# Kernel optimization log

Measured on AMD Instinct MI355X. Metric: run time of the kernel, lower is better.

Reference implementation:

```python
import jax, jax.numpy as jnp
import numpy as np

D = 768
H = 12
DH = D // H
DFF = 4 * D
B, S = 2, 2048


def setup_inputs() -> dict:
    key = jax.random.key(0)
    ks = jax.random.split(key, 12)
    inp = {
        "X": jax.random.normal(ks[0], (B, S, D), dtype=jnp.float32),
        # per-head projections, stacked over heads (nn.Linear: y = x W^T + b; we store W already transposed as [d, d_h])
        "Wq": jax.random.normal(ks[1], (H, D, DH), dtype=jnp.float32) * (1.0 / np.sqrt(D)),
        "bq": jnp.zeros((H, DH), dtype=jnp.float32),
        "Wk": jax.random.normal(ks[2], (H, D, DH), dtype=jnp.float32) * (1.0 / np.sqrt(D)),
        "bk": jnp.zeros((H, DH), dtype=jnp.float32),
        "Wv": jax.random.normal(ks[3], (H, D, DH), dtype=jnp.float32) * (1.0 / np.sqrt(D)),
        "bv": jnp.zeros((H, DH), dtype=jnp.float32),
        "W0": jax.random.normal(ks[4], (D, D), dtype=jnp.float32) * (1.0 / np.sqrt(D)),
        "b0": jnp.zeros((D,), dtype=jnp.float32),
        # FFN params are torch.randn (unit std) in the original
        "W1": jax.random.normal(ks[5], (D, DFF), dtype=jnp.float32),
        "b1": jnp.zeros((DFF,), dtype=jnp.float32),
        "W2": jax.random.normal(ks[6], (DFF, D), dtype=jnp.float32),
        "b2": jnp.zeros((D,), dtype=jnp.float32),
        "g1": jnp.ones((D,), dtype=jnp.float32),
        "o1": jnp.zeros((D,), dtype=jnp.float32),
        "g2": jnp.ones((D,), dtype=jnp.float32),
        "o2": jnp.zeros((D,), dtype=jnp.float32),
    }
    return inp


def _layernorm(x, gain, offset):
    # original: (x - mean) / (std + 1e-5)  with population std (unbiased=False)
    m = jnp.mean(x, axis=-1, keepdims=True)
    sd = jnp.sqrt(jnp.mean((x - m) ** 2, axis=-1, keepdims=True))
    return gain * ((x - m) / (sd + 1e-5)) + offset


def _mha(x, Wq, bq, Wk, bk, Wv, bv, W0, b0):
    # batched over heads; equivalent to the per-head SHA loop + concat
    q = jnp.einsum("bsd,hdk->bhsk", x, Wq) + bq[None, :, None, :]
    k = jnp.einsum("bsd,hdk->bhsk", x, Wk) + bk[None, :, None, :]
    v = jnp.einsum("bsd,hdk->bhsk", x, Wv) + bv[None, :, None, :]
    scores = jnp.einsum("bhsk,bhtk->bhst", q, k) / np.sqrt(DH).astype(np.float32)
    seq = x.shape[1]
    causal = jnp.tril(jnp.ones((seq, seq), dtype=bool))
    scores = jnp.where(causal[None, None], scores, -jnp.inf)
    w = jax.nn.softmax(scores, axis=-1)
    out = jnp.einsum("bhst,bhtk->bhsk", w, v)
    out = jnp.transpose(out, (0, 2, 1, 3)).reshape(x.shape[0], seq, D)  # concat heads
    return out @ W0 + b0


def reference(X, Wq, bq, Wk, bk, Wv, bv, W0, b0, W1, b1, W2, b2, g1, o1, g2, o2):
    h = X + _mha(_layernorm(X, g1, o1), Wq, bq, Wk, bk, Wv, bv, W0, b0)
    y = _layernorm(h, g2, o2)
    y = jnp.maximum(y @ W1 + b1, 0.0) @ W2 + b2
    return h + y
```

## Files before the change

### kernel.cpp

```cpp
#include <hip/hip_runtime.h>
#include <hip/hip_bf16.h>
#include <cstdint>

#define BB 2
#define SS 2048
#define DD 768
#define HH 12
#define DHH 64
#define DFF 3072
#define MM (BB * SS)

typedef __attribute__((ext_vector_type(8))) short bf16x8;
typedef __attribute__((ext_vector_type(4))) float f32x4;
typedef __attribute__((ext_vector_type(16))) float f32x16;
typedef __attribute__((ext_vector_type(4))) unsigned short u16x4;
typedef __attribute__((ext_vector_type(8))) unsigned short u16x8;
typedef unsigned int u32;

#define DEV static __device__ __forceinline__

typedef __attribute__((address_space(1))) void AS1void;
typedef __attribute__((address_space(3))) void AS3void;

DEV void async_copy16(const void* g, void* l) {
  __builtin_amdgcn_global_load_lds((AS1void*)g, (AS3void*)l, 16, 0, 0);
}

DEV unsigned short bf16bits(float f) {
  __hip_bfloat16 h = __float2bfloat16(f);
  return *(unsigned short*)&h;
}

DEV float bits2f(unsigned short u) {
  u32 x = ((u32)u) << 16;
  union { u32 u; float f; } c; c.u = x;
  return c.f;
}

DEV u32 pack2(float a, float b) {
  return ((u32)bf16bits(b) << 16) | (u32)bf16bits(a);
}

__global__ __launch_bounds__(256) void prolog_kernel(
    const float* __restrict__ Wq, const float* __restrict__ Wk,
    const float* __restrict__ Wv, const float* __restrict__ bq,
    const float* __restrict__ bk, const float* __restrict__ bv,
    __hip_bfloat16* __restrict__ WqkvT, float* __restrict__ qkvbias,
    const float* __restrict__ W0, const float* __restrict__ W1,
    const float* __restrict__ W2, __hip_bfloat16* __restrict__ W0T,
    __hip_bfloat16* __restrict__ W1T, __hip_bfloat16* __restrict__ W2T,
    const float* __restrict__ X, const float* __restrict__ g1,
    const float* __restrict__ o1, __hip_bfloat16* __restrict__ ln1)
{
  __shared__ float tile[64][65];
  const int bid = blockIdx.x;

  if (bid < 432) {
    const int y = bid % 12, z = bid / 12;
    const int p = z / HH, h = z - p * HH;
    const float* in = (p == 0 ? Wq : (p == 1 ? Wk : Wv)) + (size_t)h * DD * DHH;
    const int r0 = y * 64;
    if (y == 0 && threadIdx.x < DHH) {
      const float* bsrc = (p == 0 ? bq : (p == 1 ? bk : bv));
      qkvbias[p * DD + h * DHH + threadIdx.x] = bsrc[h * DHH + threadIdx.x];
    }
    for (int i = threadIdx.x; i < 4096; i += 256) {
      int r = i >> 6, c = i & 63;
      tile[r][c] = in[(size_t)(r0 + r) * DHH + c];
    }
    __syncthreads();
    for (int i = threadIdx.x; i < 4096; i += 256) {
      int c = i >> 6, r = i & 63;
      WqkvT[(size_t)(p * DD + h * DHH + c) * DD + r0 + r] = __float2bfloat16(tile[r][c]);
    }
  } else if (bid < 1728) {
    int id = bid - 432;
    const float* in; __hip_bfloat16* out; int R, C, xt, yt;
    if (id < 144)      { in = W0; out = W0T; R = DD;  C = DD;  xt = id % 12; yt = id / 12; }
    else if (id < 720) { id -= 144; in = W1; out = W1T; R = DD;  C = DFF; xt = id % 48; yt = id / 48; }
    else               { id -= 720; in = W2; out = W2T; R = DFF; C = DD;  xt = id % 12; yt = id / 12; }
    const int c0 = xt * 64, r0 = yt * 64;
    for (int i = threadIdx.x; i < 4096; i += 256) {
      int r = i >> 6, c = i & 63;
      tile[r][c] = in[(size_t)(r0 + r) * C + c0 + c];
    }
    __syncthreads();
    for (int i = threadIdx.x; i < 4096; i += 256) {
      int c = i >> 6, r = i & 63;
      out[(size_t)(c0 + c) * R + r0 + r] = __float2bfloat16(tile[r][c]);
    }
  } else {
    const int wave = threadIdx.x >> 6;
    const int lane = threadIdx.x & 63;
    const int row = (bid - 1728) * 4 + wave;
    const float* xr = X + (size_t)row * DD;

    float4 v[3];
    float s1 = 0.f, s2 = 0.f;
#pragma unroll
    for (int j = 0; j < 3; ++j) {
      v[j] = *(const float4*)(xr + (j * 64 + lane) * 4);
      s1 += v[j].x + v[j].y + v[j].z + v[j].w;
      s2 += v[j].x * v[j].x + v[j].y * v[j].y + v[j].z * v[j].z + v[j].w * v[j].w;
    }
#pragma unroll
    for (int d = 1; d < 64; d <<= 1) {
      s1 += __shfl_xor(s1, d);
      s2 += __shfl_xor(s2, d);
    }
    const float mean = s1 * (1.0f / 768.0f);
    const float var = fmaxf(s2 * (1.0f / 768.0f) - mean * mean, 0.0f);
    const float rs = 1.0f / (sqrtf(var) + 1e-5f);

    unsigned short* orow = (unsigned short*)ln1 + (size_t)row * DD;
#pragma unroll
    for (int j = 0; j < 3; ++j) {
      const int c = (j * 64 + lane) * 4;
      float4 g4 = *(const float4*)(g1 + c);
      float4 o4 = *(const float4*)(o1 + c);
      u16x4 pk;
      pk[0] = bf16bits(g4.x * ((v[j].x - mean) * rs) + o4.x);
      pk[1] = bf16bits(g4.y * ((v[j].y - mean) * rs) + o4.y);
      pk[2] = bf16bits(g4.z * ((v[j].z - mean) * rs) + o4.z);
      pk[3] = bf16bits(g4.w * ((v[j].w - mean) * rs) + o4.w);
      *(u16x4*)(orow + c) = pk;
    }
  }
}

__global__ __launch_bounds__(256) void kvimg_kernel(
    const __hip_bfloat16* __restrict__ qkv, char* __restrict__ kimg,
    char* __restrict__ vimg)
{
  __shared__ unsigned short tileK[64][72];
  __shared__ unsigned short tileV[64][72];
  const int bh = blockIdx.y;
  const int b = bh / HH, h = bh - (bh / HH) * HH;
  const int t0 = blockIdx.x * 64;
  const int HD = 3 * DD;
  const unsigned short* Kp = (const unsigned short*)qkv + (size_t)(b * SS) * HD + DD + h * DHH;
  const unsigned short* Vp = (const unsigned short*)qkv + (size_t)(b * SS) * HD + 2 * DD + h * DHH;
  char* kdst = kimg + ((size_t)bh * 32 + blockIdx.x) * 8192;
  char* vdst = vimg + ((size_t)bh * 32 + blockIdx.x) * 8192;

  for (int i = threadIdx.x; i < 512; i += 256) {
    const int r = i >> 3, c8 = (i & 7) * 8;
    *(bf16x8*)&tileK[r][c8] = *(const bf16x8*)(Kp + (size_t)(t0 + r) * HD + c8);
    *(bf16x8*)&tileV[r][c8] = *(const bf16x8*)(Vp + (size_t)(t0 + r) * HD + c8);
  }
  __syncthreads();
  for (int i = threadIdx.x; i < 512; i += 256) {
    const int f = i >> 6, l = i & 63;
    const int kc = f >> 1, half = f & 1;
    const int lc = l & 31, lh = l >> 5;
    *(bf16x8*)(kdst + i * 16) = *(const bf16x8*)&tileK[half * 32 + lc][kc * 16 + lh * 8];
    union { unsigned short u[8]; bf16x8 v; } w;
#pragma unroll
    for (int e = 0; e < 8; ++e) w.u[e] = tileV[kc * 16 + lh * 8 + e][half * 32 + lc];
    *(bf16x8*)(vdst + i * 16) = w.v;
  }
}

template<bool RELU, bool OUT_BF16, bool HAS_RES>
__global__ __launch_bounds__(256) void gemm_bt(
    const __hip_bfloat16* __restrict__ A, const __hip_bfloat16* __restrict__ BT,
    const float* __restrict__ bias, const float* __restrict__ res,
    void* __restrict__ outp, int M, int N, int K)
{
  __shared__ __hip_bfloat16 Alds[2][128 * 32];
  __shared__ __hip_bfloat16 Blds[2][128 * 32];
  const int tid = threadIdx.x;
  const int wave = tid >> 6;
  const int lane = tid & 63;
  const int fr = lane & 15, fq = lane >> 4;
  const int wr = wave >> 1, wc = wave & 1;
  const int bm = blockIdx.y * 128, bn = blockIdx.x * 128;

  const int srow = tid >> 2;
  const int scol = (tid & 3) * 8;
  const __hip_bfloat16* ag0 = A + (size_t)(bm + srow) * K + scol;
  const __hip_bfloat16* ag1 = A + (size_t)(bm + 64 + srow) * K + scol;
  const __hip_bfloat16* bg0 = BT + (size_t)(bn + srow) * K + scol;
  const __hip_bfloat16* bg1 = BT + (size_t)(bn + 64 + srow) * K + scol;
  const int so = wave * 512;

  f32x4 acc[4][4] = {};

  async_copy16(ag0, &Alds[0][so]);
  async_copy16(ag1, &Alds[0][2048 + so]);
  async_copy16(bg0, &Blds[0][so]);
  async_copy16(bg1, &Blds[0][2048 + so]);
  __syncthreads();

  const int niter = K / 32;
  for (int i = 0; i < niter; ++i) {
    const int cur = i & 1;
    if (i + 1 < niter) {
      const int k1 = (i + 1) * 32;
      async_copy16(ag0 + k1, &Alds[cur ^ 1][so]);
      async_copy16(ag1 + k1, &Alds[cur ^ 1][2048 + so]);
      async_copy16(bg0 + k1, &Blds[cur ^ 1][so]);
      async_copy16(bg1 + k1, &Blds[cur ^ 1][2048 + so]);
    }
    bf16x8 af[4], bfr[4];
#pragma unroll
    for (int i4 = 0; i4 < 4; ++i4)
      af[i4] = *(const bf16x8*)(&Alds[cur][(wr * 64 + i4 * 16 + fr) * 32 + fq * 8]);
#pragma unroll
    for (int j4 = 0; j4 < 4; ++j4)
      bfr[j4] = *(const bf16x8*)(&Blds[cur][(wc * 64 + j4 * 16 + fr) * 32 + fq * 8]);
#pragma unroll
    for (int i4 = 0; i4 < 4; ++i4)
#pragma unroll
      for (int j4 = 0; j4 < 4; ++j4)
        acc[i4][j4] = __builtin_amdgcn_mfma_f32_16x16x32_bf16(af[i4], bfr[j4], acc[i4][j4], 0, 0, 0);
    __syncthreads();
  }

#pragma unroll
  for (int j = 0; j < 4; ++j) {
    const int c = bn + wc * 64 + j * 16 + fr;
    const float bv = bias[c];
#pragma unroll
    for (int i = 0; i < 4; ++i) {
#pragma unroll
      for (int r = 0; r < 4; ++r) {
        const int rr = bm + wr * 64 + i * 16 + fq * 4 + r;
        float v = acc[i][j][r] + bv;
        if (RELU) v = fmaxf(v, 0.0f);
        if (HAS_RES) v += res[(size_t)rr * N + c];
        if (OUT_BF16) ((__hip_bfloat16*)outp)[(size_t)rr * N + c] = __float2bfloat16(v);
        else          ((float*)outp)[(size_t)rr * N + c] = v;
      }
    }
  }
}

__global__ __launch_bounds__(256) void gemm_bt_sk(
    const __hip_bfloat16* __restrict__ A, const __hip_bfloat16* __restrict__ BT,
    unsigned short* __restrict__ part01, unsigned short* __restrict__ part23,
    int M, int N, int K, int K_per)
{
  __shared__ __hip_bfloat16 Alds[2][128 * 32];
  __shared__ __hip_bfloat16 Blds[2][128 * 32];
  const int tid = threadIdx.x;
  const int wave = tid >> 6;
  const int lane = tid & 63;
  const int fr = lane & 15, fq = lane >> 4;
  const int wr = wave >> 1, wc = wave & 1;
  const int bm = blockIdx.y * 128, bn = blockIdx.x * 128;
  const int z = blockIdx.z;
  unsigned short* part = (z < 2 ? part01 : part23) + (size_t)(z & 1) * M * N;
  const int kbase = z * K_per;

  const int srow = tid >> 2;
  const int scol = (tid & 3) * 8;
  const __hip_bfloat16* ag0 = A + (size_t)(bm + srow) * K + scol + kbase;
  const __hip_bfloat16* ag1 = A + (size_t)(bm + 64 + srow) * K + scol + kbase;
  const __hip_bfloat16* bg0 = BT + (size_t)(bn + srow) * K + scol + kbase;
  const __hip_bfloat16* bg1 = BT + (size_t)(bn + 64 + srow) * K + scol + kbase;
  const int so = wave * 512;

  f32x4 acc[4][4] = {};

  async_copy16(ag0, &Alds[0][so]);
  async_copy16(ag1, &Alds[0][2048 + so]);
  async_copy16(bg0, &Blds[0][so]);
  async_copy16(bg1, &Blds[0][2048 + so]);
  __syncthreads();

  const int niter = K_per / 32;
  for (int i = 0; i < niter; ++i) {
    const int cur = i & 1;
    if (i + 1 < niter) {
      const int k1 = (i + 1) * 32;
      async_copy16(ag0 + k1, &Alds[cur ^ 1][so]);
      async_copy16(ag1 + k1, &Alds[cur ^ 1][2048 + so]);
      async_copy16(bg0 + k1, &Blds[cur ^ 1][so]);
      async_copy16(bg1 + k1, &Blds[cur ^ 1][2048 + so]);
    }
    bf16x8 af[4], bfr[4];
#pragma unroll
    for (int i4 = 0; i4 < 4; ++i4)
      af[i4] = *(const bf16x8*)(&Alds[cur][(wr * 64 + i4 * 16 + fr) * 32 + fq * 8]);
#pragma unroll
    for (int j4 = 0; j4 < 4; ++j4)
      bfr[j4] = *(const bf16x8*)(&Blds[cur][(wc * 64 + j4 * 16 + fr) * 32 + fq * 8]);
#pragma unroll
    for (int i4 = 0; i4 < 4; ++i4)
#pragma unroll
      for (int j4 = 0; j4 < 4; ++j4)
        acc[i4][j4] = __builtin_amdgcn_mfma_f32_16x16x32_bf16(af[i4], bfr[j4], acc[i4][j4], 0, 0, 0);
    __syncthreads();
  }

#pragma unroll
  for (int j = 0; j < 4; ++j) {
    const int c = bn + wc * 64 + j * 16 + fr;
#pragma unroll
    for (int i = 0; i < 4; ++i) {
#pragma unroll
      for (int r = 0; r < 4; ++r) {
        const int rr = bm + wr * 64 + i * 16 + fq * 4 + r;
        part[(size_t)rr * N + c] = bf16bits(acc[i][j][r]);
      }
    }
  }
}

__global__ __launch_bounds__(256) void combine4(
    const unsigned short* __restrict__ part01, const unsigned short* __restrict__ part23,
    const float* __restrict__ res, const float* __restrict__ bias,
    float* __restrict__ out, int MN, int N)
{
  const int idx = (blockIdx.x * 256 + threadIdx.x) * 4;
  if (idx >= MN) return;
  const u16x4 a0 = *(const u16x4*)(part01 + idx);
  const u16x4 a1 = *(const u16x4*)(part01 + MN + idx);
  const u16x4 a2 = *(const u16x4*)(part23 + idx);
  const u16x4 a3 = *(const u16x4*)(part23 + MN + idx);
  const float4 rr = *(const float4*)(res + idx);
  const float4 bb = *(const float4*)(bias + (idx % N));
  float4 o;
  o.x = bits2f(a0[0]) + bits2f(a1[0]) + bits2f(a2[0]) + bits2f(a3[0]) + rr.x + bb.x;
  o.y = bits2f(a0[1]) + bits2f(a1[1]) + bits2f(a2[1]) + bits2f(a3[1]) + rr.y + bb.y;
  o.z = bits2f(a0[2]) + bits2f(a1[2]) + bits2f(a2[2]) + bits2f(a3[2]) + rr.z + bb.z;
  o.w = bits2f(a0[3]) + bits2f(a1[3]) + bits2f(a2[3]) + bits2f(a3[3]) + rr.w + bb.w;
  *(float4*)(out + idx) = o;
}

__global__ __launch_bounds__(256) void combine2_ln(
    const unsigned short* __restrict__ part, const float* __restrict__ res,
    const float* __restrict__ bias, const float* __restrict__ gain,
    const float* __restrict__ off, float* __restrict__ hout,
    __hip_bfloat16* __restrict__ lnout)
{
  const int wave = threadIdx.x >> 6;
  const int lane = threadIdx.x & 63;
  const int row = blockIdx.x * 4 + wave;
  const int MN = MM * DD;
  const size_t rbase = (size_t)row * DD;

  float v[3][4];
  float s1 = 0.f, s2 = 0.f;
#pragma unroll
  for (int j = 0; j < 3; ++j) {
    const int c = (j * 64 + lane) * 4;
    const size_t idx = rbase + c;
    const u16x4 a0 = *(const u16x4*)(part + idx);
    const u16x4 a1 = *(const u16x4*)(part + MN + idx);
    const float4 rr = *(const float4*)(res + idx);
    const float4 bb = *(const float4*)(bias + c);
    v[j][0] = bits2f(a0[0]) + bits2f(a1[0]) + rr.x + bb.x;
    v[j][1] = bits2f(a0[1]) + bits2f(a1[1]) + rr.y + bb.y;
    v[j][2] = bits2f(a0[2]) + bits2f(a1[2]) + rr.z + bb.z;
    v[j][3] = bits2f(a0[3]) + bits2f(a1[3]) + rr.w + bb.w;
    float4 hv = { v[j][0], v[j][1], v[j][2], v[j][3] };
    *(float4*)(hout + idx) = hv;
    s1 += v[j][0] + v[j][1] + v[j][2] + v[j][3];
    s2 += v[j][0]*v[j][0] + v[j][1]*v[j][1] + v[j][2]*v[j][2] + v[j][3]*v[j][3];
  }
#pragma unroll
  for (int d = 1; d < 64; d <<= 1) {
    s1 += __shfl_xor(s1, d);
    s2 += __shfl_xor(s2, d);
  }
  const float mean = s1 * (1.0f / 768.0f);
  const float var = fmaxf(s2 * (1.0f / 768.0f) - mean * mean, 0.0f);
  const float rs = 1.0f / (sqrtf(var) + 1e-5f);

  unsigned short* orow = (unsigned short*)lnout + rbase;
#pragma unroll
  for (int j = 0; j < 3; ++j) {
    const int c = (j * 64 + lane) * 4;
    const float4 g4 = *(const float4*)(gain + c);
    const float4 o4 = *(const float4*)(off + c);
    u16x4 pk;
    pk[0] = bf16bits(g4.x * ((v[j][0] - mean) * rs) + o4.x);
    pk[1] = bf16bits(g4.y * ((v[j][1] - mean) * rs) + o4.y);
    pk[2] = bf16bits(g4.z * ((v[j][2] - mean) * rs) + o4.z);
    pk[3] = bf16bits(g4.w * ((v[j][3] - mean) * rs) + o4.w);
    *(u16x4*)(orow + c) = pk;
  }
}

__global__ __launch_bounds__(128, 3) void attn_kernel(
    const __hip_bfloat16* __restrict__ qkv, const char* __restrict__ kimg,
    const char* __restrict__ vimg, __hip_bfloat16* __restrict__ outp)
{
  const int HD = 3 * DD;
  const int id = blockIdx.x;
  const int xcd = id & 7;
  const int j = id >> 3;
  const int s2 = 63 - j / 3;
  const int bhl = j - 3 * (j / 3);
  const int bh = xcd * 3 + bhl;
  const int b = bh / HH, h = bh - (bh / HH) * HH;

  const int q0w = s2 * 32;
  const int tid = threadIdx.x;
  const int c = tid >> 6;
  const int lane = tid & 63;
  const int col = lane & 31, hi = lane >> 5;
  const int qg = q0w + col;

  const size_t base = (size_t)b * SS * HD;
  const __hip_bfloat16* Qp = qkv + base + h * DHH;
  const char* kimg_h = kimg + (size_t)bh * 32 * 8192;
  const char* vimg_h = vimg + (size_t)bh * 32 * 8192;

  __shared__ __align__(16) char sm[17408];

  bf16x8 qf[4];
#pragma unroll
  for (int kc = 0; kc < 4; ++kc)
    qf[kc] = *(const bf16x8*)(Qp + (size_t)qg * HD + kc * 16 + hi * 8);

  f32x16 o0 = {}, o1 = {};
  float mreg = -1e30f, lreg = 0.f;
  const float CS = 0.125f * 1.44269504f;

  const int ntiles = (q0w >> 6) + 1;

  bf16x8 kf[8];
  {
    const char* ks = kimg_h + (size_t)c * 8192 + lane * 16;
#pragma unroll
    for (int f = 0; f < 8; ++f) kf[f] = *(const bf16x8*)(ks + f * 1024);
  }

  for (int t = c; t < ntiles; t += 2) {
    const int kv0 = t * 64;
    f32x16 s0 = {}, s1 = {};
    __builtin_amdgcn_s_setprio(1);
#pragma unroll
    for (int kc = 0; kc < 4; ++kc) {
      s0 = __builtin_amdgcn_mfma_f32_32x32x16_bf16(kf[kc * 2],     qf[kc], s0, 0, 0, 0);
      s1 = __builtin_amdgcn_mfma_f32_32x32x16_bf16(kf[kc * 2 + 1], qf[kc], s1, 0, 0, 0);
    }
    __builtin_amdgcn_s_setprio(0);
    bf16x8 vf[8];
    {
      const char* vs = vimg_h + (size_t)t * 8192 + lane * 16;
#pragma unroll
      for (int f = 0; f < 8; ++f) vf[f] = *(const bf16x8*)(vs + f * 1024);
    }
    if (t + 2 < ntiles) {
      const char* ks = kimg_h + (size_t)(t + 2) * 8192 + lane * 16;
#pragma unroll
      for (int f = 0; f < 8; ++f) kf[f] = *(const bf16x8*)(ks + f * 1024);
    }
    if (kv0 + 63 > q0w) {
#pragma unroll
      for (int r = 0; r < 16; ++r) {
        const int tl = (r & 3) + 8 * (r >> 2) + 4 * hi;
        s0[r] = (kv0 + tl <= qg) ? s0[r] : -1e30f;
        s1[r] = (kv0 + 32 + tl <= qg) ? s1[r] : -1e30f;
      }
    }
    float mx = s0[0];
#pragma unroll
    for (int r = 1; r < 16; ++r) mx = fmaxf(mx, s0[r]);
#pragma unroll
    for (int r = 0; r < 16; ++r) mx = fmaxf(mx, s1[r]);
    mx = fmaxf(mx, __shfl_xor(mx, 32));
    const float mnew = fmaxf(mreg, mx);
    const float alpha = exp2f((mreg - mnew) * CS);
    mreg = mnew;
    const float mc = mnew * CS;
    float ps = 0.f;
#pragma unroll
    for (int r = 0; r < 16; ++r) {
      const float p0 = exp2f(s0[r] * CS - mc); s0[r] = p0; ps += p0;
      const float p1 = exp2f(s1[r] * CS - mc); s1[r] = p1; ps += p1;
    }
    ps += __shfl_xor(ps, 32);
    lreg = lreg * alpha + ps;
#pragma unroll
    for (int r = 0; r < 16; ++r) { o0[r] *= alpha; o1[r] *= alpha; }

    u32 pk0[4][2], pk1[4][2];
#pragma unroll
    for (int qd = 0; qd < 4; ++qd) {
      pk0[qd][0] = pack2(s0[4 * qd + 0], s0[4 * qd + 1]);
      pk0[qd][1] = pack2(s0[4 * qd + 2], s0[4 * qd + 3]);
      pk1[qd][0] = pack2(s1[4 * qd + 0], s1[4 * qd + 1]);
      pk1[qd][1] = pack2(s1[4 * qd + 2], s1[4 * qd + 3]);
    }
#pragma unroll
    for (int kc = 0; kc < 4; ++kc) {
      const int qa = 2 * (kc & 1), qb = qa + 1;
      const u32 A0 = (kc < 2) ? pk0[qa][0] : pk1[qa][0];
      const u32 A1 = (kc < 2) ? pk0[qa][1] : pk1[qa][1];
      const u32 B0 = (kc < 2) ? pk0[qb][0] : pk1[qb][0];
      const u32 B1 = (kc < 2) ? pk0[qb][1] : pk1[qb][1];
      const u32 send0 = hi ? A0 : B0;
      const u32 send1 = hi ? A1 : B1;
      const u32 recv0 = __shfl_xor(send0, 32);
      const u32 recv1 = __shfl_xor(send1, 32);
      const u32 su0 = hi ? B0 : A0;
      const u32 su1 = hi ? B1 : A1;
      union { u32 u[4]; bf16x8 v; } pf;
      pf.u[0] = hi ? recv0 : su0;
      pf.u[1] = hi ? recv1 : su1;
      pf.u[2] = hi ? su0 : recv0;
      pf.u[3] = hi ? su1 : recv1;
      __builtin_amdgcn_s_setprio(1);
      o0 = __builtin_amdgcn_mfma_f32_32x32x16_bf16(vf[kc * 2],     pf.v, o0, 0, 0, 0);
      o1 = __builtin_amdgcn_mfma_f32_32x32x16_bf16(vf[kc * 2 + 1], pf.v, o1, 0, 0, 0);
      __builtin_amdgcn_s_setprio(0);
    }
  }

  float* opart = (float*)sm;
  float* mlp   = (float*)(sm + 16640);
#pragma unroll
  for (int r = 0; r < 16; ++r) {
    const int d = (r & 3) + 8 * (r >> 2) + 4 * hi;
    opart[(c * 32 + col) * 65 + d]      = o0[r];
    opart[(c * 32 + col) * 65 + d + 32] = o1[r];
  }
  if (hi == 0) {
    mlp[c * 64 + col]      = mreg;
    mlp[c * 64 + 32 + col] = lreg;
  }
  __syncthreads();

  const int q = tid >> 2;
  const int d0 = (tid & 3) * 16;
  float mcv[2], lcv[2];
#pragma unroll
  for (int cc = 0; cc < 2; ++cc) {
    mcv[cc] = mlp[cc * 64 + q];
    lcv[cc] = mlp[cc * 64 + 32 + q];
  }
  const float mstar = fmaxf(mcv[0], mcv[1]);
  float av[2], lstar = 0.f;
#pragma unroll
  for (int cc = 0; cc < 2; ++cc) {
    av[cc] = exp2f((mcv[cc] - mstar) * CS);
    lstar += av[cc] * lcv[cc];
  }
  const float inv = 1.0f / lstar;
  float acc[16] = {};
#pragma unroll
  for (int cc = 0; cc < 2; ++cc) {
    const float a = av[cc];
#pragma unroll
    for (int e = 0; e < 16; ++e)
      acc[e] += a * opart[(cc * 32 + q) * 65 + d0 + e];
  }
  unsigned short* orow = (unsigned short*)outp +
      (size_t)(b * SS + q0w + q) * DD + h * DHH + d0;
  u16x8 w8;
#pragma unroll
  for (int e = 0; e < 8; ++e) w8[e] = bf16bits(acc[e] * inv);
  *(u16x8*)orow = w8;
#pragma unroll
  for (int e = 0; e < 8; ++e) w8[e] = bf16bits(acc[8 + e] * inv);
  *(u16x8*)(orow + 8) = w8;
}

extern "C" void kernel_launch(void* const* d_in, const int* in_sizes, int n_in,
                              void* d_out, int out_size, void* d_ws, size_t ws_size,
                              hipStream_t stream)
{
  (void)in_sizes; (void)n_in; (void)out_size; (void)ws_size;
  const float* X  = (const float*)d_in[0];
  const float* Wq = (const float*)d_in[1];
  const float* bq = (const float*)d_in[2];
  const float* Wk = (const float*)d_in[3];
  const float* bk = (const float*)d_in[4];
  const float* Wv = (const float*)d_in[5];
  const float* bv = (const float*)d_in[6];
  const float* W0 = (const float*)d_in[7];
  const float* b0 = (const float*)d_in[8];
  const float* W1 = (const float*)d_in[9];
  const float* b1 = (const float*)d_in[10];
  const float* W2 = (const float*)d_in[11];
  const float* b2 = (const float*)d_in[12];
  const float* g1 = (const float*)d_in[13];
  const float* o1 = (const float*)d_in[14];
  const float* g2 = (const float*)d_in[15];
  const float* o2 = (const float*)d_in[16];

  char* ws = (char*)d_ws;
  auto alloc = [&](size_t bytes) {
    char* p = ws;
    ws += (bytes + 255) & ~(size_t)255;
    return p;
  };
  __hip_bfloat16* ln1    = (__hip_bfloat16*)alloc((size_t)MM * DD * 2);
  __hip_bfloat16* qkvb16 = (__hip_bfloat16*)alloc((size_t)MM * 3 * DD * 2);
  __hip_bfloat16* attnb  = (__hip_bfloat16*)alloc((size_t)MM * DD * 2);
  float*          hbuf   = (float*)alloc((size_t)MM * DD * 4);
  __hip_bfloat16* ln2    = (__hip_bfloat16*)alloc((size_t)MM * DD * 2);
  __hip_bfloat16* ffn1   = (__hip_bfloat16*)alloc((size_t)MM * DFF * 2);
  __hip_bfloat16* WqkvT  = (__hip_bfloat16*)alloc((size_t)3 * DD * DD * 2);
  __hip_bfloat16* W0T    = (__hip_bfloat16*)alloc((size_t)DD * DD * 2);
  __hip_bfloat16* W1T    = (__hip_bfloat16*)alloc((size_t)DFF * DD * 2);
  __hip_bfloat16* W2T    = (__hip_bfloat16*)alloc((size_t)DD * DFF * 2);
  float*          qkvbias= (float*)alloc((size_t)3 * DD * 4);
  unsigned short* part23 = (unsigned short*)alloc((size_t)2 * MM * DD * 2);
  char*           kimg   = alloc((size_t)24 * 32 * 8192);
  char*           vimg   = alloc((size_t)24 * 32 * 8192);
  unsigned short* part01 = (unsigned short*)ln1;

  prolog_kernel<<<2752, 256, 0, stream>>>(
      Wq, Wk, Wv, bq, bk, bv, WqkvT, qkvbias,
      W0, W1, W2, W0T, W1T, W2T,
      X, g1, o1, ln1);

  gemm_bt<false, true, false><<<dim3(3 * DD / 128, MM / 128), 256, 0, stream>>>(
      ln1, WqkvT, qkvbias, nullptr, qkvb16, MM, 3 * DD, DD);
  kvimg_kernel<<<dim3(SS / 64, BB * HH), 256, 0, stream>>>(qkvb16, kimg, vimg);
  attn_kernel<<<1536, 128, 0, stream>>>(qkvb16, kimg, vimg, attnb);
  gemm_bt_sk<<<dim3(DD / 128, MM / 128, 2), 256, 0, stream>>>(
      attnb, W0T, part23, part23, MM, DD, DD, DD / 2);
  combine2_ln<<<MM / 4, 256, 0, stream>>>(
      part23, X, b0, g2, o2, hbuf, ln2);
  gemm_bt<true, true, false><<<dim3(DFF / 128, MM / 128), 256, 0, stream>>>(
      ln2, W1T, b1, nullptr, ffn1, MM, DFF, DD);
  gemm_bt_sk<<<dim3(DD / 128, MM / 128, 4), 256, 0, stream>>>(
      ffn1, W2T, part01, part23, MM, DD, DFF, DFF / 4);
  combine4<<<(MM * DD) / 1024, 256, 0, stream>>>(
      part01, part23, hbuf, b2, (float*)d_out, MM * DD, DD);
}
```

Measured before the change: 178.1 us.

## Fuse K/V image relayout into QKV GEMM epilogue, drop kvimg kernel

Adds a dedicated QKV GEMM whose epilogue writes Q into a compact Q buffer and scatters K and V directly into the MFMA-friendly image layouts the attention kernel reads. The separate kvimg relayout kernel and the full QKV intermediate round trip through memory go away, saving one launch and the extra reads and writes. The cost is scattered 2-byte stores in the epilogue, which may coalesce poorly.

```diff
diff --git a/kernel.cpp b/kernel.cpp
--- a/kernel.cpp
+++ b/kernel.cpp
@@ -128,36 +128,120 @@
   }
 }
 
-__global__ __launch_bounds__(256) void kvimg_kernel(
-    const __hip_bfloat16* __restrict__ qkv, char* __restrict__ kimg,
-    char* __restrict__ vimg)
+__global__ __launch_bounds__(256) void gemm_qkv(
+    const __hip_bfloat16* __restrict__ A, const __hip_bfloat16* __restrict__ BT,
+    const float* __restrict__ bias, __hip_bfloat16* __restrict__ qbuf,
+    char* __restrict__ kimg, char* __restrict__ vimg)
 {
-  __shared__ unsigned short tileK[64][72];
-  __shared__ unsigned short tileV[64][72];
-  const int bh = blockIdx.y;
-  const int b = bh / HH, h = bh - (bh / HH) * HH;
-  const int t0 = blockIdx.x * 64;
-  const int HD = 3 * DD;
-  const unsigned short* Kp = (const unsigned short*)qkv + (size_t)(b * SS) * HD + DD + h * DHH;
-  const unsigned short* Vp = (const unsigned short*)qkv + (size_t)(b * SS) * HD + 2 * DD + h * DHH;
-  char* kdst = kimg + ((size_t)bh * 32 + blockIdx.x) * 8192;
-  char* vdst = vimg + ((size_t)bh * 32 + blockIdx.x) * 8192;
-
-  for (int i = threadIdx.x; i < 512; i += 256) {
-    const int r = i >> 3, c8 = (i & 7) * 8;
-    *(bf16x8*)&tileK[r][c8] = *(const bf16x8*)(Kp + (size_t)(t0 + r) * HD + c8);
-    *(bf16x8*)&tileV[r][c8] = *(const bf16x8*)(Vp + (size_t)(t0 + r) * HD + c8);
-  }
+  const int K = DD;
+  __shared__ __hip_bfloat16 Alds[2][128 * 32];
+  __shared__ __hip_bfloat16 Blds[2][128 * 32];
+  const int tid = threadIdx.x;
+  const int wave = tid >> 6;
+  const int lane = tid & 63;
+  const int fr = lane & 15, fq = lane >> 4;
+  const int wr = wave >> 1, wc = wave & 1;
+  const int bm = blockIdx.y * 128, bn = blockIdx.x * 128;
+
+  const int srow = tid >> 2;
+  const int scol = (tid & 3) * 8;
+  const __hip_bfloat16* ag0 = A + (size_t)(bm + srow) * K + scol;
+  const __hip_bfloat16* ag1 = A + (size_t)(bm + 64 + srow) * K + scol;
+  const __hip_bfloat16* bg0 = BT + (size_t)(bn + srow) * K + scol;
+  const __hip_bfloat16* bg1 = BT + (size_t)(bn + 64 + srow) * K + scol;
+  const int so = wave * 512;
+
+  f32x4 acc[4][4] = {};
+
+  async_copy16(ag0, &Alds[0][so]);
+  async_copy16(ag1, &Alds[0][2048 + so]);
+  async_copy16(bg0, &Blds[0][so]);
+  async_copy16(bg1, &Blds[0][2048 + so]);
   __syncthreads();
-  for (int i = threadIdx.x; i < 512; i += 256) {
-    const int f = i >> 6, l = i & 63;
-    const int kc = f >> 1, half = f & 1;
-    const int lc = l & 31, lh = l >> 5;
-    *(bf16x8*)(kdst + i * 16) = *(const bf16x8*)&tileK[half * 32 + lc][kc * 16 + lh * 8];
-    union { unsigned short u[8]; bf16x8 v; } w;
-#pragma unroll
-    for (int e = 0; e < 8; ++e) w.u[e] = tileV[kc * 16 + lh * 8 + e][half * 32 + lc];
-    *(bf16x8*)(vdst + i * 16) = w.v;
+
+  const int niter = K / 32;
+  for (int i = 0; i < niter; ++i) {
+    const int cur = i & 1;
+    if (i + 1 < niter) {
+      const int k1 = (i + 1) * 32;
+      async_copy16(ag0 + k1, &Alds[cur ^ 1][so]);
+      async_copy16(ag1 + k1, &Alds[cur ^ 1][2048 + so]);
+      async_copy16(bg0 + k1, &Blds[cur ^ 1][so]);
+      async_copy16(bg1 + k1, &Blds[cur ^ 1][2048 + so]);
+    }
+    bf16x8 af[4], bfr[4];
+#pragma unroll
+    for (int i4 = 0; i4 < 4; ++i4)
+      af[i4] = *(const bf16x8*)(&Alds[cur][(wr * 64 + i4 * 16 + fr) * 32 + fq * 8]);
+#pragma unroll
+    for (int j4 = 0; j4 < 4; ++j4)
+      bfr[j4] = *(const bf16x8*)(&Blds[cur][(wc * 64 + j4 * 16 + fr) * 32 + fq * 8]);
+#pragma unroll
+    for (int i4 = 0; i4 < 4; ++i4)
+#pragma unroll
+      for (int j4 = 0; j4 < 4; ++j4)
+        acc[i4][j4] = __builtin_amdgcn_mfma_f32_16x16x32_bf16(af[i4], bfr[j4], acc[i4][j4], 0, 0, 0);
+    __syncthreads();
+  }
+
+  if (bn < DD) {
+#pragma unroll
+    for (int j = 0; j < 4; ++j) {
+      const int c = bn + wc * 64 + j * 16 + fr;
+      const float bv = bias[c];
+#pragma unroll
+      for (int i = 0; i < 4; ++i) {
+#pragma unroll
+        for (int r = 0; r < 4; ++r) {
+          const int rr = bm + wr * 64 + i * 16 + fq * 4 + r;
+          ((unsigned short*)qbuf)[(size_t)rr * DD + c] = bf16bits(acc[i][j][r] + bv);
+        }
+      }
+    }
+  } else if (bn < 2 * DD) {
+    const int h = (bn - DD + wc * 64) >> 6;
+#pragma unroll
+    for (int j = 0; j < 4; ++j) {
+      const int c = bn + wc * 64 + j * 16 + fr;
+      const float bv = bias[c];
+      const int dk = j * 16 + fr;
+      const int kc = dk >> 4, lh = (dk >> 3) & 1, e = dk & 7;
+#pragma unroll
+      for (int i = 0; i < 4; ++i) {
+#pragma unroll
+        for (int r = 0; r < 4; ++r) {
+          const int rr = bm + wr * 64 + i * 16 + fq * 4 + r;
+          const int b = rr >> 11, t = (rr >> 6) & 31, rk = rr & 63;
+          const int half = rk >> 5, lc = rk & 31;
+          const int ii = (kc * 2 + half) * 64 + lh * 32 + lc;
+          unsigned short* dst = (unsigned short*)(kimg +
+              ((size_t)((b * HH + h) * 32 + t)) * 8192);
+          dst[ii * 8 + e] = bf16bits(acc[i][j][r] + bv);
+        }
+      }
+    }
+  } else {
+    const int h = (bn - 2 * DD + wc * 64) >> 6;
+#pragma unroll
+    for (int j = 0; j < 4; ++j) {
+      const int c = bn + wc * 64 + j * 16 + fr;
+      const float bv = bias[c];
+      const int dv = j * 16 + fr;
+      const int half = dv >> 5, lc = dv & 31;
+#pragma unroll
+      for (int i = 0; i < 4; ++i) {
+#pragma unroll
+        for (int r = 0; r < 4; ++r) {
+          const int rr = bm + wr * 64 + i * 16 + fq * 4 + r;
+          const int b = rr >> 11, t = (rr >> 6) & 31, rv = rr & 63;
+          const int kc = rv >> 4, lh = (rv >> 3) & 1, e = rv & 7;
+          const int ii = (kc * 2 + half) * 64 + lh * 32 + lc;
+          unsigned short* dst = (unsigned short*)(vimg +
+              ((size_t)((b * HH + h) * 32 + t)) * 8192);
+          dst[ii * 8 + e] = bf16bits(acc[i][j][r] + bv);
+        }
+      }
+    }
   }
 }
 
@@ -385,10 +469,9 @@
 }
 
 __global__ __launch_bounds__(128, 3) void attn_kernel(
-    const __hip_bfloat16* __restrict__ qkv, const char* __restrict__ kimg,
+    const __hip_bfloat16* __restrict__ qbuf, const char* __restrict__ kimg,
     const char* __restrict__ vimg, __hip_bfloat16* __restrict__ outp)
 {
-  const int HD = 3 * DD;
   const int id = blockIdx.x;
   const int xcd = id & 7;
   const int j = id >> 3;
@@ -404,8 +487,7 @@
   const int col = lane & 31, hi = lane >> 5;
   const int qg = q0w + col;
 
-  const size_t base = (size_t)b * SS * HD;
-  const __hip_bfloat16* Qp = qkv + base + h * DHH;
+  const __hip_bfloat16* Qp = qbuf + (size_t)b * SS * DD + h * DHH;
   const char* kimg_h = kimg + (size_t)bh * 32 * 8192;
   const char* vimg_h = vimg + (size_t)bh * 32 * 8192;
 
@@ -414,7 +496,7 @@
   bf16x8 qf[4];
 #pragma unroll
   for (int kc = 0; kc < 4; ++kc)
-    qf[kc] = *(const bf16x8*)(Qp + (size_t)qg * HD + kc * 16 + hi * 8);
+    qf[kc] = *(const bf16x8*)(Qp + (size_t)qg * DD + kc * 16 + hi * 8);
 
   f32x16 o0 = {}, o1 = {};
   float mreg = -1e30f, lreg = 0.f;
@@ -591,7 +673,7 @@
     return p;
   };
   __hip_bfloat16* ln1    = (__hip_bfloat16*)alloc((size_t)MM * DD * 2);
-  __hip_bfloat16* qkvb16 = (__hip_bfloat16*)alloc((size_t)MM * 3 * DD * 2);
+  __hip_bfloat16* qbuf   = (__hip_bfloat16*)alloc((size_t)MM * DD * 2);
   __hip_bfloat16* attnb  = (__hip_bfloat16*)alloc((size_t)MM * DD * 2);
   float*          hbuf   = (float*)alloc((size_t)MM * DD * 4);
   __hip_bfloat16* ln2    = (__hip_bfloat16*)alloc((size_t)MM * DD * 2);
@@ -611,10 +693,9 @@
       W0, W1, W2, W0T, W1T, W2T,
       X, g1, o1, ln1);
 
-  gemm_bt<false, true, false><<<dim3(3 * DD / 128, MM / 128), 256, 0, stream>>>(
-      ln1, WqkvT, qkvbias, nullptr, qkvb16, MM, 3 * DD, DD);
-  kvimg_kernel<<<dim3(SS / 64, BB * HH), 256, 0, stream>>>(qkvb16, kimg, vimg);
-  attn_kernel<<<1536, 128, 0, stream>>>(qkvb16, kimg, vimg, attnb);
+  gemm_qkv<<<dim3(3 * DD / 128, MM / 128), 256, 0, stream>>>(
+      ln1, WqkvT, qkvbias, qbuf, kimg, vimg);
+  attn_kernel<<<1536, 128, 0, stream>>>(qbuf, kimg, vimg, attnb);
   gemm_bt_sk<<<dim3(DD / 128, MM / 128, 2), 256, 0, stream>>>(
       attnb, W0T, part23, part23, MM, DD, DD, DD / 2);
   combine2_ln<<<MM / 4, 256, 0, stream>>>(
```

Measured after the change: 192.3 us. 7.9% more time.
